# Kernel tuning notes

Measured on AMD Instinct MI355X. Metric: run time of the kernel, lower is better.

The kernel has to match this reference:

```python
import jax, jax.numpy as jnp
import numpy as np

B = 100_000   # graph nodes in batch
C = 1_000     # virtual-node clusters
D = 512       # in_dim (attention hidden dim)
OUT = 512     # out_dim


def setup_inputs() -> dict:
    key = jax.random.key(0)
    ks = jax.random.split(key, 9)
    h = jax.random.normal(ks[0], (B, D), dtype=jnp.float32)
    g = jax.random.normal(ks[1], (C, D), dtype=jnp.float32)
    # vn_index[:,1] is the cluster id of node i; arange%C guarantees every
    # cluster is present, so the per-cluster concat has exactly C rows in
    # sorted-cluster-id order (matching torch .unique() iteration order).
    vn_index = jnp.stack([jnp.arange(B, dtype=jnp.int32),
                          jnp.arange(B, dtype=jnp.int32) % C], axis=1)
    n_id = jnp.arange(B, dtype=jnp.int32)
    s = 1.0 / np.sqrt(D)
    Wq = jax.random.uniform(ks[2], (D, D), jnp.float32, -s, s)   # query_proj (no bias)
    Wk = jax.random.uniform(ks[3], (D, D), jnp.float32, -s, s)   # key_proj (no bias)
    attn_bias = jax.random.uniform(ks[4], (D,), jnp.float32, -0.1, 0.1)
    Ws = jax.random.uniform(ks[5], (1, D), jnp.float32, -s, s)   # score_proj weight
    bs = jax.random.uniform(ks[6], (1,), jnp.float32, -s, s)     # score_proj bias
    so = 1.0 / np.sqrt(D)
    W = jax.random.uniform(ks[7], (OUT, D), jnp.float32, -so, so)  # final Linear
    b = jax.random.uniform(ks[8], (OUT,), jnp.float32, -so, so)
    return {"h": h, "g": g, "vn_index": vn_index, "n_id": n_id,
            "Wq": Wq, "Wk": Wk, "attn_bias": attn_bias, "Ws": Ws, "bs": bs,
            "W": W, "b": b}


def reference(h, g, vn_index, n_id, Wq, Wk, attn_bias, Ws, bs, W, b):
    # cluster id for each batch node (B,)
    cluster = vn_index[n_id, 1]
    # additive attention, vectorized over all nodes (replaces per-cluster loop)
    qp = g @ Wq.T                                   # (C, D) query proj per cluster
    kp = h @ Wk.T                                   # (B, D) key proj per node
    score = jnp.tanh(kp + qp[cluster] + attn_bias) @ Ws[0] + bs[0]  # (B,)
    # segment softmax over each cluster
    smax = jax.ops.segment_max(score, cluster, num_segments=C)      # (C,)
    e = jnp.exp(score - smax[cluster])                              # (B,)
    denom = jax.ops.segment_sum(e, cluster, num_segments=C)         # (C,)
    attn = e / denom[cluster]                                       # (B,)
    # attention-weighted sum of node features per cluster -> (C, D)
    ctx = jax.ops.segment_sum(attn[:, None] * h, cluster, num_segments=C)
    # final projection + tanh activation -> (C, OUT)
    return jnp.tanh(ctx @ W.T + b)
```

## Files before the change

### kernel.cpp

```cpp
#include <hip/hip_runtime.h>
#include <stdint.h>

#define D_DIM 512

typedef __attribute__((ext_vector_type(8))) short bf16x8;
typedef __attribute__((ext_vector_type(4))) float f32x4;
typedef __attribute__((ext_vector_type(4))) short short4_t;
typedef __attribute__((ext_vector_type(4))) float float4_t;

__device__ __forceinline__ unsigned short f2bf(float f) {
  unsigned u = __float_as_uint(f);
  u += 0x7FFFu + ((u >> 16) & 1u);
  return (unsigned short)(u >> 16);
}

__device__ __forceinline__ float bf2f(unsigned short s) {
  return __uint_as_float(((unsigned)s) << 16);
}

__device__ __forceinline__ float tanh_fast(float x) {
  float e = __expf(2.0f * x);
  return 1.0f - 2.0f / (e + 1.0f);
}

#define GLOAD_LDS16(gsrc, ldst) \
  __builtin_amdgcn_global_load_lds((const __attribute__((address_space(1))) void*)(gsrc), \
                                   (__attribute__((address_space(3))) void*)(ldst), 16, 0, 0)


__global__ void cvt_f32_bf16_k(const float* __restrict__ in, unsigned short* __restrict__ out, int n4) {
  int i = blockIdx.x * blockDim.x + threadIdx.x;
  if (i < n4) {
    float4_t v = ((const float4_t*)in)[i];
    short4_t s;
    s.x = (short)f2bf(v.x); s.y = (short)f2bf(v.y);
    s.z = (short)f2bf(v.z); s.w = (short)f2bf(v.w);
    ((short4_t*)out)[i] = s;
  }
}

__global__ void cvt3_f32_bf16_k(const float* __restrict__ a, const float* __restrict__ b,
                                const float* __restrict__ c, unsigned short* __restrict__ out,
                                int n4each) {
  int i = blockIdx.x * blockDim.x + threadIdx.x;
  if (i >= 3 * n4each) return;
  int sel = i / n4each, j = i - sel * n4each;
  const float* src = (sel == 0) ? a : (sel == 1) ? b : c;
  float4_t v = ((const float4_t*)src)[j];
  short4_t s;
  s.x = (short)f2bf(v.x); s.y = (short)f2bf(v.y);
  s.z = (short)f2bf(v.z); s.w = (short)f2bf(v.w);
  ((short4_t*)out)[i] = s;
}

__global__ void prep_cluster_k(const int* __restrict__ vn, const int* __restrict__ nid,
                               int* __restrict__ cl, int* __restrict__ counts, int B) {
  int i = blockIdx.x * blockDim.x + threadIdx.x;
  if (i < B) {
    int c = vn[2 * nid[i] + 1];
    cl[i] = c;
    atomicAdd(&counts[c], 1);
  }
}

__global__ void prefix_k(const int* __restrict__ counts, int* __restrict__ starts,
                         int* __restrict__ cursor, int C) {
  __shared__ int sh[1024];
  int t = threadIdx.x;
  int v = (t < C) ? counts[t] : 0;
  sh[t] = v;
  __syncthreads();
  for (int off = 1; off < 1024; off <<= 1) {
    int x = (t >= off) ? sh[t - off] : 0;
    __syncthreads();
    sh[t] += x;
    __syncthreads();
  }
  if (t < C) { int st = sh[t] - v; starts[t] = st; cursor[t] = st; }
  if (t == 1023) starts[C] = sh[1023];
}

__global__ void scatter_k(const int* __restrict__ cl, int* __restrict__ cursor,
                          int* __restrict__ order, int B) {
  int i = blockIdx.x * blockDim.x + threadIdx.x;
  if (i < B) {
    int pos = atomicAdd(&cursor[cl[i]], 1);
    order[pos] = i;
  }
}

__device__ __forceinline__ unsigned enc_f(float f) {
  unsigned u = __float_as_uint(f);
  return (u & 0x80000000u) ? ~u : (u | 0x80000000u);
}
__device__ __forceinline__ float dec_f(unsigned u) {
  return __uint_as_float((u & 0x80000000u) ? (u & 0x7FFFFFFFu) : ~u);
}

__global__ void seg_max_k(const float* __restrict__ score, const int* __restrict__ cl,
                          unsigned* __restrict__ smax, int B) {
  int i = blockIdx.x * blockDim.x + threadIdx.x;
  if (i < B) atomicMax(&smax[cl[i]], enc_f(score[i]));
}

__global__ void seg_expsum_k(const float* __restrict__ score, const int* __restrict__ cl,
                             const unsigned* __restrict__ smax, float* __restrict__ ev,
                             float* __restrict__ denom, int B) {
  int i = blockIdx.x * blockDim.x + threadIdx.x;
  if (i < B) {
    int c = cl[i];
    float x = __expf(score[i] - dec_f(smax[c]));
    ev[i] = x;
    atomicAdd(&denom[c], x);
  }
}

__global__ __launch_bounds__(256)
void ctx_k(const unsigned short* __restrict__ hbf, const float* __restrict__ ev,
           const int* __restrict__ order, const int* __restrict__ starts,
           const float* __restrict__ denom, float* __restrict__ ctx) {
  int c = blockIdx.x;
  int t = threadIdx.x;
  int s0 = starts[c], s1 = starts[c + 1];
  float a0 = 0.f, a1 = 0.f;
  int j = s0;
  for (; j + 3 < s1; j += 4) {
    int i0 = order[j], i1 = order[j + 1], i2 = order[j + 2], i3 = order[j + 3];
    float e0 = ev[i0], e1 = ev[i1], e2 = ev[i2], e3 = ev[i3];
    unsigned u0 = *(const unsigned*)(hbf + (size_t)i0 * D_DIM + t * 2);
    unsigned u1 = *(const unsigned*)(hbf + (size_t)i1 * D_DIM + t * 2);
    unsigned u2 = *(const unsigned*)(hbf + (size_t)i2 * D_DIM + t * 2);
    unsigned u3 = *(const unsigned*)(hbf + (size_t)i3 * D_DIM + t * 2);
    a0 += e0 * bf2f((unsigned short)u0) + e1 * bf2f((unsigned short)u1)
        + e2 * bf2f((unsigned short)u2) + e3 * bf2f((unsigned short)u3);
    a1 += e0 * bf2f((unsigned short)(u0 >> 16)) + e1 * bf2f((unsigned short)(u1 >> 16))
        + e2 * bf2f((unsigned short)(u2 >> 16)) + e3 * bf2f((unsigned short)(u3 >> 16));
  }
  for (; j < s1; ++j) {
    int i0 = order[j];
    float e0 = ev[i0];
    unsigned u0 = *(const unsigned*)(hbf + (size_t)i0 * D_DIM + t * 2);
    a0 += e0 * bf2f((unsigned short)u0);
    a1 += e0 * bf2f((unsigned short)(u0 >> 16));
  }
  float inv = 1.0f / denom[c];
  float2 r = make_float2(a0 * inv, a1 * inv);
  *(float2*)(&ctx[(size_t)c * D_DIM + t * 2]) = r;
}

template<int EPI>
__global__ __launch_bounds__(256)
void gemm128_k(const unsigned short* __restrict__ Abf,
               const unsigned short* __restrict__ Bw, int M,
               const float* __restrict__ qb, const int* __restrict__ cl,
               const float* __restrict__ Ws, const float* __restrict__ bias,
               float* __restrict__ out)
{
  __shared__ unsigned short As[2][128 * 64];
  __shared__ unsigned short Bs[2][128 * 64];
  __shared__ float red[128][2];
  __shared__ int clds[128];

  const int t = threadIdx.x;
  const int lane = t & 63;
  const int w = t >> 6;
  const int wr = w >> 1, wc = w & 1;
  const int l15 = lane & 15, l4 = lane >> 4;

  const int nwg = gridDim.x;
  int id = blockIdx.x;
  if ((nwg & 7) == 0) id = (id & 7) * (nwg >> 3) + (id >> 3);
  const int n0 = (id & 3) * 128;
  const int m0 = (id >> 2) * 128;

  if (EPI == 1 && t < 128) {
    int gm = m0 + t;
    clds[t] = (gm < M) ? cl[gm] : 0;
  }

  const int rin = lane >> 3;
  const int sl = lane & 7;

  const unsigned short* srcA[4];
  const unsigned short* srcB[4];
  int dstOff[4];
  #pragma unroll
  for (int c = 0; c < 4; ++c) {
    int chunk = w * 4 + c;
    int row = chunk * 8 + rin;
    int slot = sl ^ (row & 7);
    int ga = m0 + row; if (ga > M - 1) ga = M - 1;
    srcA[c] = Abf + (size_t)ga * 512 + slot * 8;
    srcB[c] = Bw + (size_t)(n0 + row) * 512 + slot * 8;
    dstOff[c] = chunk * 1024;
  }

  int offA[4][2], offB[4][2];
  #pragma unroll
  for (int mi = 0; mi < 4; ++mi) {
    int row = wr * 64 + mi * 16 + l15;
    #pragma unroll
    for (int ks = 0; ks < 2; ++ks)
      offA[mi][ks] = row * 128 + (((ks * 4 + l4) ^ (row & 7)) * 16);
  }
  #pragma unroll
  for (int ni = 0; ni < 4; ++ni) {
    int row = wc * 64 + ni * 16 + l15;
    #pragma unroll
    for (int ks = 0; ks < 2; ++ks)
      offB[ni][ks] = row * 128 + (((ks * 4 + l4) ^ (row & 7)) * 16);
  }

  f32x4 acc[4][4];
  #pragma unroll
  for (int mi = 0; mi < 4; ++mi)
    #pragma unroll
    for (int ni = 0; ni < 4; ++ni)
      acc[mi][ni] = (f32x4){0.f, 0.f, 0.f, 0.f};

  #pragma unroll
  for (int c = 0; c < 4; ++c) {
    GLOAD_LDS16(srcA[c], ((char*)As[0]) + dstOff[c]);
    GLOAD_LDS16(srcB[c], ((char*)Bs[0]) + dstOff[c]);
  }
  __syncthreads();

  #pragma unroll
  for (int it = 0; it < 8; ++it) {
    const int cur = it & 1;
    if (it < 7) {
      const int k1 = (it + 1) * 64;
      #pragma unroll
      for (int c = 0; c < 4; ++c) {
        GLOAD_LDS16(srcA[c] + k1, ((char*)As[cur ^ 1]) + dstOff[c]);
        GLOAD_LDS16(srcB[c] + k1, ((char*)Bs[cur ^ 1]) + dstOff[c]);
      }
    }
    #pragma unroll
    for (int ks = 0; ks < 2; ++ks) {
      bf16x8 af[4], bfv[4];
      #pragma unroll
      for (int mi = 0; mi < 4; ++mi)
        af[mi] = *(const bf16x8*)(((const char*)As[cur]) + offA[mi][ks]);
      #pragma unroll
      for (int ni = 0; ni < 4; ++ni)
        bfv[ni] = *(const bf16x8*)(((const char*)Bs[cur]) + offB[ni][ks]);
      #pragma unroll
      for (int mi = 0; mi < 4; ++mi)
        #pragma unroll
        for (int ni = 0; ni < 4; ++ni)
          acc[mi][ni] = __builtin_amdgcn_mfma_f32_16x16x32_bf16(af[mi], bfv[ni], acc[mi][ni], 0, 0, 0);
    }
    __syncthreads();
  }

  if (EPI == 0 || EPI == 2) {
    #pragma unroll
    for (int mi = 0; mi < 4; ++mi) {
      #pragma unroll
      for (int r = 0; r < 4; ++r) {
        int gm = m0 + wr * 64 + mi * 16 + l4 * 4 + r;
        if (gm < M) {
          #pragma unroll
          for (int ni = 0; ni < 4; ++ni) {
            int gcol = n0 + wc * 64 + ni * 16 + l15;
            float v = acc[mi][ni][r] + bias[gcol];
            if (EPI == 2) v = tanh_fast(v);
            out[(size_t)gm * 512 + gcol] = v;
          }
        }
      }
    }
  } else {
    #pragma unroll
    for (int mi = 0; mi < 4; ++mi) {
      #pragma unroll
      for (int r = 0; r < 4; ++r) {
        int rowt = wr * 64 + mi * 16 + l4 * 4 + r;
        int c = clds[rowt];
        const float* qrow = &qb[(size_t)c * 512 + n0 + wc * 64];
        float s = 0.f;
        #pragma unroll
        for (int ni = 0; ni < 4; ++ni) {
          int colw = ni * 16 + l15;
          float x = acc[mi][ni][r] + qrow[colw];
          s += tanh_fast(x) * Ws[n0 + wc * 64 + colw];
        }
        s += __shfl_xor(s, 1);
        s += __shfl_xor(s, 2);
        s += __shfl_xor(s, 4);
        s += __shfl_xor(s, 8);
        if (l15 == 0) red[rowt][wc] = s;
      }
    }
    __syncthreads();
    if (t < 128) {
      int gm = m0 + t;
      if (gm < M) atomicAdd(&out[gm], red[t][0] + red[t][1]);
    }
  }
}


extern "C" void kernel_launch(void* const* d_in, const int* in_sizes, int n_in,
                              void* d_out, int out_size, void* d_ws, size_t ws_size,
                              hipStream_t stream) {
  const float* h  = (const float*)d_in[0];
  const float* g  = (const float*)d_in[1];
  const int*   vn = (const int*)d_in[2];
  const int*   nid= (const int*)d_in[3];
  const float* Wq = (const float*)d_in[4];
  const float* Wk = (const float*)d_in[5];
  const float* ab = (const float*)d_in[6];
  const float* Ws = (const float*)d_in[7];
  const float* W  = (const float*)d_in[9];
  const float* b  = (const float*)d_in[10];

  const int B = in_sizes[3];
  const int C = in_sizes[1] / D_DIM;

  char* wsb = (char*)d_ws;
  size_t off = 0;
  auto alloc = [&](size_t bytes) -> void* {
    void* p = wsb + off;
    off += (bytes + 255) & ~(size_t)255;
    return p;
  };

  unsigned short* hbf   = (unsigned short*)alloc((size_t)B * 512 * 2);
  unsigned short* gbf   = (unsigned short*)alloc((size_t)C * 512 * 2);
  unsigned short* ctxbf = (unsigned short*)alloc((size_t)C * 512 * 2);
  unsigned short* Wk_bf = (unsigned short*)alloc((size_t)512 * 512 * 2);
  unsigned short* Wq_bf = (unsigned short*)alloc((size_t)512 * 512 * 2);
  unsigned short* W_bf  = (unsigned short*)alloc((size_t)512 * 512 * 2);
  float* qb    = (float*)alloc((size_t)C * 512 * 4);
  float* ctx   = (float*)alloc((size_t)C * 512 * 4);
  float* score = (float*)alloc((size_t)B * 4);
  float* ev    = (float*)alloc((size_t)B * 4);
  int*   cl    = (int*)alloc((size_t)B * 4);
  int*   order = (int*)alloc((size_t)B * 4);
  int*      counts = (int*)alloc((size_t)C * 4);
  unsigned* smax   = (unsigned*)alloc((size_t)C * 4);
  float*    denom  = (float*)alloc((size_t)C * 4);
  int* starts = (int*)alloc((size_t)(C + 1) * 4);
  int* cursor = (int*)alloc((size_t)C * 4);
  (void)ws_size; (void)n_in; (void)out_size;

  size_t zlen = (size_t)((char*)denom - (char*)counts) + (size_t)C * 4;
  hipMemsetAsync(counts, 0, zlen, stream);
  hipMemsetAsync(score, 0, (size_t)B * 4, stream);

  cvt_f32_bf16_k<<<(B * 512 / 4 + 255) / 256, 256, 0, stream>>>(h, hbf, B * 512 / 4);
  cvt_f32_bf16_k<<<(C * 512 / 4 + 255) / 256, 256, 0, stream>>>(g, gbf, C * 512 / 4);
  const int n4w = 512 * 512 / 4;
  cvt3_f32_bf16_k<<<(3 * n4w + 255) / 256, 256, 0, stream>>>(Wk, Wq, W, Wk_bf, n4w);

  prep_cluster_k<<<(B + 255) / 256, 256, 0, stream>>>(vn, nid, cl, counts, B);
  prefix_k<<<1, 1024, 0, stream>>>(counts, starts, cursor, C);
  scatter_k<<<(B + 255) / 256, 256, 0, stream>>>(cl, cursor, order, B);

  gemm128_k<0><<<4 * ((C + 127) / 128), 256, 0, stream>>>(
      gbf, Wq_bf, C, nullptr, nullptr, nullptr, ab, qb);

  gemm128_k<1><<<4 * ((B + 127) / 128), 256, 0, stream>>>(
      hbf, Wk_bf, B, qb, cl, Ws, nullptr, score);

  seg_max_k<<<(B + 255) / 256, 256, 0, stream>>>(score, cl, smax, B);
  seg_expsum_k<<<(B + 255) / 256, 256, 0, stream>>>(score, cl, smax, ev, denom, B);
  ctx_k<<<C, 256, 0, stream>>>(hbf, ev, order, starts, denom, ctx);

  cvt_f32_bf16_k<<<(C * 512 / 4 + 255) / 256, 256, 0, stream>>>(ctx, ctxbf, C * 512 / 4);

  gemm128_k<2><<<4 * ((C + 127) / 128), 256, 0, stream>>>(
      ctxbf, W_bf, C, nullptr, nullptr, nullptr, b, (float*)d_out);
}
```

Measured before the change: 261.9 us.

## Load GEMM operands directly into registers instead of staging through LDS

Replaces the LDS double-buffered GEMM, which filled shared memory with global_load_lds, with a version where each lane loads its MFMA fragments straight from global memory into registers, double-buffered across 16 k-steps of 32. Removing the per-iteration barriers and most LDS use lets three blocks per CU run (launch_bounds 256,3). The cost is that fragments shared between waves are no longer reused on-chip, so each wave fetches its own A and B rows, which raises global and L2 traffic. Those loads are also 16 bytes per lane with a row stride, so they are less coalesced.

```diff
diff --git a/kernel.cpp b/kernel.cpp
--- a/kernel.cpp
+++ b/kernel.cpp
@@ -22,10 +22,6 @@
   float e = __expf(2.0f * x);
   return 1.0f - 2.0f / (e + 1.0f);
 }
-
-#define GLOAD_LDS16(gsrc, ldst) \
-  __builtin_amdgcn_global_load_lds((const __attribute__((address_space(1))) void*)(gsrc), \
-                                   (__attribute__((address_space(3))) void*)(ldst), 16, 0, 0)
 
 
 __global__ void cvt_f32_bf16_k(const float* __restrict__ in, unsigned short* __restrict__ out, int n4) {
@@ -149,18 +145,13 @@
 }
 
 template<int EPI>
-__global__ __launch_bounds__(256)
-void gemm128_k(const unsigned short* __restrict__ Abf,
-               const unsigned short* __restrict__ Bw, int M,
-               const float* __restrict__ qb, const int* __restrict__ cl,
-               const float* __restrict__ Ws, const float* __restrict__ bias,
-               float* __restrict__ out)
+__global__ __launch_bounds__(256, 3)
+void gemm128_reg_k(const unsigned short* __restrict__ Abf,
+                   const unsigned short* __restrict__ Bw, int M,
+                   const float* __restrict__ qb, const int* __restrict__ cl,
+                   const float* __restrict__ Ws, const float* __restrict__ bias,
+                   float* __restrict__ out)
 {
-  __shared__ unsigned short As[2][128 * 64];
-  __shared__ unsigned short Bs[2][128 * 64];
-  __shared__ float red[128][2];
-  __shared__ int clds[128];
-
   const int t = threadIdx.x;
   const int lane = t & 63;
   const int w = t >> 6;
@@ -173,42 +164,17 @@
   const int n0 = (id & 3) * 128;
   const int m0 = (id >> 2) * 128;
 
-  if (EPI == 1 && t < 128) {
-    int gm = m0 + t;
-    clds[t] = (gm < M) ? cl[gm] : 0;
-  }
-
-  const int rin = lane >> 3;
-  const int sl = lane & 7;
-
-  const unsigned short* srcA[4];
-  const unsigned short* srcB[4];
-  int dstOff[4];
-  #pragma unroll
-  for (int c = 0; c < 4; ++c) {
-    int chunk = w * 4 + c;
-    int row = chunk * 8 + rin;
-    int slot = sl ^ (row & 7);
-    int ga = m0 + row; if (ga > M - 1) ga = M - 1;
-    srcA[c] = Abf + (size_t)ga * 512 + slot * 8;
-    srcB[c] = Bw + (size_t)(n0 + row) * 512 + slot * 8;
-    dstOff[c] = chunk * 1024;
-  }
-
-  int offA[4][2], offB[4][2];
+  const unsigned short* aP[4];
+  const unsigned short* bP[4];
   #pragma unroll
   for (int mi = 0; mi < 4; ++mi) {
-    int row = wr * 64 + mi * 16 + l15;
-    #pragma unroll
-    for (int ks = 0; ks < 2; ++ks)
-      offA[mi][ks] = row * 128 + (((ks * 4 + l4) ^ (row & 7)) * 16);
+    int row = m0 + wr * 64 + mi * 16 + l15; if (row > M - 1) row = M - 1;
+    aP[mi] = Abf + (size_t)row * 512 + l4 * 8;
   }
   #pragma unroll
   for (int ni = 0; ni < 4; ++ni) {
-    int row = wc * 64 + ni * 16 + l15;
-    #pragma unroll
-    for (int ks = 0; ks < 2; ++ks)
-      offB[ni][ks] = row * 128 + (((ks * 4 + l4) ^ (row & 7)) * 16);
+    int col = n0 + wc * 64 + ni * 16 + l15;
+    bP[ni] = Bw + (size_t)col * 512 + l4 * 8;
   }
 
   f32x4 acc[4][4];
@@ -218,40 +184,27 @@
     for (int ni = 0; ni < 4; ++ni)
       acc[mi][ni] = (f32x4){0.f, 0.f, 0.f, 0.f};
 
-  #pragma unroll
-  for (int c = 0; c < 4; ++c) {
-    GLOAD_LDS16(srcA[c], ((char*)As[0]) + dstOff[c]);
-    GLOAD_LDS16(srcB[c], ((char*)Bs[0]) + dstOff[c]);
-  }
-  __syncthreads();
-
-  #pragma unroll
-  for (int it = 0; it < 8; ++it) {
-    const int cur = it & 1;
-    if (it < 7) {
-      const int k1 = (it + 1) * 64;
-      #pragma unroll
-      for (int c = 0; c < 4; ++c) {
-        GLOAD_LDS16(srcA[c] + k1, ((char*)As[cur ^ 1]) + dstOff[c]);
-        GLOAD_LDS16(srcB[c] + k1, ((char*)Bs[cur ^ 1]) + dstOff[c]);
-      }
+  bf16x8 af[2][4], bfv[2][4];
+  #pragma unroll
+  for (int mi = 0; mi < 4; ++mi) af[0][mi] = *(const bf16x8*)(aP[mi]);
+  #pragma unroll
+  for (int ni = 0; ni < 4; ++ni) bfv[0][ni] = *(const bf16x8*)(bP[ni]);
+
+  #pragma unroll
+  for (int it = 0; it < 16; ++it) {
+    const int cur = it & 1, nxt = cur ^ 1;
+    if (it < 15) {
+      const int k1 = (it + 1) * 32;
+      #pragma unroll
+      for (int mi = 0; mi < 4; ++mi) af[nxt][mi] = *(const bf16x8*)(aP[mi] + k1);
+      #pragma unroll
+      for (int ni = 0; ni < 4; ++ni) bfv[nxt][ni] = *(const bf16x8*)(bP[ni] + k1);
     }
     #pragma unroll
-    for (int ks = 0; ks < 2; ++ks) {
-      bf16x8 af[4], bfv[4];
-      #pragma unroll
-      for (int mi = 0; mi < 4; ++mi)
-        af[mi] = *(const bf16x8*)(((const char*)As[cur]) + offA[mi][ks]);
+    for (int mi = 0; mi < 4; ++mi)
       #pragma unroll
       for (int ni = 0; ni < 4; ++ni)
-        bfv[ni] = *(const bf16x8*)(((const char*)Bs[cur]) + offB[ni][ks]);
-      #pragma unroll
-      for (int mi = 0; mi < 4; ++mi)
-        #pragma unroll
-        for (int ni = 0; ni < 4; ++ni)
-          acc[mi][ni] = __builtin_amdgcn_mfma_f32_16x16x32_bf16(af[mi], bfv[ni], acc[mi][ni], 0, 0, 0);
-    }
-    __syncthreads();
+        acc[mi][ni] = __builtin_amdgcn_mfma_f32_16x16x32_bf16(af[cur][mi], bfv[cur][ni], acc[mi][ni], 0, 0, 0);
   }
 
   if (EPI == 0 || EPI == 2) {
@@ -272,6 +225,13 @@
       }
     }
   } else {
+    __shared__ float red[128][2];
+    __shared__ int clds[128];
+    if (t < 128) {
+      int gm = m0 + t;
+      clds[t] = (gm < M) ? cl[gm] : 0;
+    }
+    __syncthreads();
     #pragma unroll
     for (int mi = 0; mi < 4; ++mi) {
       #pragma unroll
@@ -359,10 +319,10 @@
   prefix_k<<<1, 1024, 0, stream>>>(counts, starts, cursor, C);
   scatter_k<<<(B + 255) / 256, 256, 0, stream>>>(cl, cursor, order, B);
 
-  gemm128_k<0><<<4 * ((C + 127) / 128), 256, 0, stream>>>(
+  gemm128_reg_k<0><<<4 * ((C + 127) / 128), 256, 0, stream>>>(
       gbf, Wq_bf, C, nullptr, nullptr, nullptr, ab, qb);
 
-  gemm128_k<1><<<4 * ((B + 127) / 128), 256, 0, stream>>>(
+  gemm128_reg_k<1><<<4 * ((B + 127) / 128), 256, 0, stream>>>(
       hbf, Wk_bf, B, qb, cl, Ws, nullptr, score);
 
   seg_max_k<<<(B + 255) / 256, 256, 0, stream>>>(score, cl, smax, B);
@@ -371,6 +331,6 @@
 
   cvt_f32_bf16_k<<<(C * 512 / 4 + 255) / 256, 256, 0, stream>>>(ctx, ctxbf, C * 512 / 4);
 
-  gemm128_k<2><<<4 * ((C + 127) / 128), 256, 0, stream>>>(
+  gemm128_reg_k<2><<<4 * ((C + 127) / 128), 256, 0, stream>>>(
       ctxbf, W_bf, C, nullptr, nullptr, nullptr, b, (float*)d_out);
 }
```

Result: slower. 381.4 us (+45.7%).
